# Performance work log

Measured on AMD Instinct MI355X. Metric: run time of the kernel, lower is better.

The kernel has to match this reference:

```python
import jax, jax.numpy as jnp
import numpy as np

N = 10000          # nodes
E = 320000         # edges (avg degree 32)
D_IN = 64          # node_pos feature width
NS, NG, NV = 128, 128, 128   # gate: scalars, gates, gated channels
NTYPES = 8         # edge types
FC = 64            # fc_neurons hidden width
D_OUT = 64
NUM_NEIGHBORS = 32.0


def setup_inputs() -> dict:
    key = jax.random.key(0)
    ks = jax.random.split(key, 32)
    inp = {}
    inp["node_pos"] = jax.random.normal(ks[0], (N, D_IN), dtype=jnp.float32)
    dims_in = [D_IN, D_IN + NS + NV, D_IN + NS + NV]     # 64, 320, 320
    dims_out = [NS + NG + NV, NS + NG + NV, D_OUT]       # 384, 384, 64
    i = 1
    for l in range(3):
        di, do = dims_in[l], dims_out[l]
        inp[f"w_self_{l}"] = jax.random.normal(ks[i], (di, do), dtype=jnp.float32) / np.sqrt(di); i += 1
        inp[f"w_msg_{l}"] = jax.random.normal(ks[i], (di, do), dtype=jnp.float32) / np.sqrt(di); i += 1
        inp[f"fc0_{l}"] = jax.random.normal(ks[i], (NTYPES, FC), dtype=jnp.float32) / np.sqrt(NTYPES); i += 1
        inp[f"fc1_{l}"] = jax.random.normal(ks[i], (FC, FC), dtype=jnp.float32) / np.sqrt(FC); i += 1
        inp[f"fc2_{l}"] = jax.random.normal(ks[i], (FC, do), dtype=jnp.float32) / np.sqrt(FC); i += 1
    inp["edge_src"] = jax.random.randint(ks[i], (E,), 0, N); i += 1
    inp["edge_dst"] = jax.random.randint(ks[i], (E,), 0, N); i += 1
    inp["edge_type"] = jax.random.randint(ks[i], (E,), 0, NTYPES)
    return inp


def _conv(x, edge_src, edge_dst, etype_onehot, w_self, w_msg, f0, f1, f2):
    # fc_neurons MLP on edge attrs -> per-edge tensor-product weights [E, out]
    w = jax.nn.silu(etype_onehot @ f0)
    w = jax.nn.silu(w @ f1)
    w = w @ f2
    # gather source node features, weighted message, scatter-sum to dst
    msg = (x[edge_src] @ w_msg) * w                       # [E, out]
    agg = jax.ops.segment_sum(msg, edge_dst, num_segments=N)
    agg = agg / jnp.sqrt(jnp.asarray(NUM_NEIGHBORS, x.dtype))
    return x @ w_self + agg                               # self-connection + messages


def _gate(h):
    # e3nn Gate: scalars -> silu, gates -> sigmoid, gated channels modulated by gates
    s = h[:, :NS]
    g = h[:, NS:NS + NG]
    v = h[:, NS + NG:]
    return jnp.concatenate([jax.nn.silu(s), v * jax.nn.sigmoid(g)], axis=-1)


def reference(node_pos,
              w_self_0, w_msg_0, fc0_0, fc1_0, fc2_0,
              w_self_1, w_msg_1, fc0_1, fc1_1, fc2_1,
              w_self_2, w_msg_2, fc0_2, fc1_2, fc2_2,
              edge_src, edge_dst, edge_type):
    etype_onehot = jax.nn.one_hot(edge_type, NTYPES, dtype=node_pos.dtype)
    mid = node_pos
    params = [(w_self_0, w_msg_0, fc0_0, fc1_0, fc2_0),
              (w_self_1, w_msg_1, fc0_1, fc1_1, fc2_1)]
    for w_self, w_msg, f0, f1, f2 in params:
        h = _conv(mid, edge_src, edge_dst, etype_onehot, w_self, w_msg, f0, f1, f2)
        mid = jnp.concatenate([node_pos, _gate(h)], axis=-1)   # concated_tensor
    return _conv(mid, edge_src, edge_dst, etype_onehot, w_self_2, w_msg_2, fc0_2, fc1_2, fc2_2)
```

## Files before the change

### kernel.cpp

```cpp
#include <hip/hip_runtime.h>
#include <hip/hip_bf16.h>

#define N_NODES 10000
#define N_EDGES 320000
#define NTYPES 8
#define FC 64
#define SLOTS 96

using short8v = __attribute__((ext_vector_type(8))) short;
using f32x4   = __attribute__((ext_vector_type(4))) float;

__device__ __forceinline__ float sigmoidf_(float x) { return 1.f / (1.f + expf(-x)); }

__device__ __forceinline__ unsigned short f2bf(float x) {
    union { float f; unsigned u; } un; un.f = x;
    unsigned r = un.u + 0x7fff + ((un.u >> 16) & 1);
    return (unsigned short)(r >> 16);
}
__device__ __forceinline__ float bf2f(unsigned short b) {
    union { unsigned u; float f; } un; un.u = ((unsigned)b) << 16;
    return un.f;
}
__device__ __forceinline__ float bflo(unsigned d) {
    union { unsigned u; float f; } un; un.u = d << 16; return un.f;
}
__device__ __forceinline__ float bfhi(unsigned d) {
    union { unsigned u; float f; } un; un.u = d & 0xffff0000u; return un.f;
}
__device__ __forceinline__ unsigned packbf(float lo, float hi) {
    return (unsigned)f2bf(lo) | ((unsigned)f2bf(hi) << 16);
}

__device__ __forceinline__ void wtrans(const float* __restrict__ in,
                                       unsigned short* __restrict__ out,
                                       int K, int Nn, int idx) {
    int n = idx / K, k = idx - n * K;
    out[idx] = f2bf(in[k * Nn + n]);
}

__global__ void prep_misc(const float* __restrict__ node_pos,
                          const float* __restrict__ w0, const float* __restrict__ w1,
                          const float* __restrict__ w2, const float* __restrict__ w3,
                          const float* __restrict__ w4, const float* __restrict__ w5,
                          int* __restrict__ cnt, unsigned short* __restrict__ np16,
                          unsigned short* __restrict__ o0, unsigned short* __restrict__ o1,
                          unsigned short* __restrict__ o2, unsigned short* __restrict__ o3,
                          unsigned short* __restrict__ o4, unsigned short* __restrict__ o5) {
    int idx = blockIdx.x * 256 + threadIdx.x;
    if (idx < N_NODES) { cnt[idx] = 0; return; }
    idx -= N_NODES;
    if (idx < N_NODES * 64) { np16[idx] = f2bf(node_pos[idx]); return; }
    idx -= N_NODES * 64;
    if (idx < 24576) { wtrans(w0, o0, 64, 384, idx); return; }
    idx -= 24576;
    if (idx < 24576) { wtrans(w1, o1, 64, 384, idx); return; }
    idx -= 24576;
    if (idx < 122880) { wtrans(w2, o2, 320, 384, idx); return; }
    idx -= 122880;
    if (idx < 122880) { wtrans(w3, o3, 320, 384, idx); return; }
    idx -= 122880;
    if (idx < 20480) { wtrans(w4, o4, 320, 64, idx); return; }
    idx -= 20480;
    if (idx < 20480) { wtrans(w5, o5, 320, 64, idx); return; }
}
#define PREP_TOTAL (N_NODES + N_NODES * 64 + 2 * 24576 + 2 * 122880 + 2 * 20480)

__global__ void fill_kernel(const int* __restrict__ esrc, const int* __restrict__ edst,
                            const int* __restrict__ etype, int* __restrict__ cnt,
                            int* __restrict__ csr) {
    int e = blockIdx.x * 256 + threadIdx.x;
    if (e >= N_EDGES) return;
    int d = edst[e];
    int pos = atomicAdd(&cnt[d], 1);
    if (pos < SLOTS) csr[d * SLOTS + pos] = esrc[e] * 8 + etype[e];
}

__global__ void wtab_fused(const float* __restrict__ f0_0, const float* __restrict__ f1_0,
                           const float* __restrict__ f2_0,
                           const float* __restrict__ f0_1, const float* __restrict__ f1_1,
                           const float* __restrict__ f2_1,
                           const float* __restrict__ f0_2, const float* __restrict__ f1_2,
                           const float* __restrict__ f2_2,
                           float* __restrict__ wtab0, float* __restrict__ wtab1,
                           float* __restrict__ wtab2) {
    const int tid = threadIdx.x;
    const int bb = blockIdx.x;
    const float *f0, *f1, *f2;
    float* wtab;
    int dout, idx;
    if (bb < 12)      { f0 = f0_0; f1 = f1_0; f2 = f2_0; wtab = wtab0; dout = 384; idx = bb * 256 + tid; }
    else if (bb < 24) { f0 = f0_1; f1 = f1_1; f2 = f2_1; wtab = wtab1; dout = 384; idx = (bb - 12) * 256 + tid; }
    else              { f0 = f0_2; f1 = f1_2; f2 = f2_2; wtab = wtab2; dout = 64;  idx = (bb - 24) * 256 + tid; }
    __shared__ float a[NTYPES * FC];
    __shared__ float bs[NTYPES * FC];
    for (int i = tid; i < NTYPES * FC; i += 256) { float v = f0[i]; a[i] = v * sigmoidf_(v); }
    __syncthreads();
    for (int i = tid; i < NTYPES * FC; i += 256) {
        int t = i >> 6, j = i & 63;
        float s = 0.f;
        #pragma unroll
        for (int k = 0; k < FC; ++k) s = fmaf(a[t * FC + k], f1[k * FC + j], s);
        bs[i] = s * sigmoidf_(s);
    }
    __syncthreads();
    if (idx >= NTYPES * dout) return;
    int t = idx / dout, c = idx - t * dout;
    float s = 0.f;
    #pragma unroll
    for (int k = 0; k < FC; ++k) s = fmaf(bs[t * FC + k], f2[k * dout + c], s);
    wtab[idx] = s * 0.17677669529663687f;
}

__global__ __launch_bounds__(256) void mfma_dual(
        const unsigned short* __restrict__ A,
        const unsigned short* __restrict__ BtS, const unsigned short* __restrict__ BtM,
        float* __restrict__ Cs, unsigned short* __restrict__ Cm,
        int M, int K, int N, int nct) {
    int by = blockIdx.y;
    const bool is_msg = (by >= nct);
    const unsigned short* Bt = is_msg ? BtM : BtS;
    if (is_msg) by -= nct;
    const int wave = threadIdx.x >> 6;
    const int lane = threadIdx.x & 63;
    const int r16 = lane & 15;
    const int kg  = lane >> 4;
    const int rowBase = blockIdx.x * 128 + wave * 32;
    const int colBase = by * 64;

    f32x4 acc[2][4] = {};
    for (int k0 = 0; k0 < K; k0 += 32) {
        short8v a[2], b[4];
        #pragma unroll
        for (int mi = 0; mi < 2; ++mi) {
            int r = rowBase + mi * 16 + r16;
            if (r >= M) r = M - 1;
            a[mi] = *reinterpret_cast<const short8v*>(&A[(long long)r * K + k0 + kg * 8]);
        }
        #pragma unroll
        for (int nj = 0; nj < 4; ++nj) {
            int c = colBase + nj * 16 + r16;
            b[nj] = *reinterpret_cast<const short8v*>(&Bt[(long long)c * K + k0 + kg * 8]);
        }
        #pragma unroll
        for (int mi = 0; mi < 2; ++mi)
            #pragma unroll
            for (int nj = 0; nj < 4; ++nj)
                acc[mi][nj] = __builtin_amdgcn_mfma_f32_16x16x32_bf16(
                                  a[mi], b[nj], acc[mi][nj], 0, 0, 0);
    }
    #pragma unroll
    for (int mi = 0; mi < 2; ++mi) {
        #pragma unroll
        for (int j = 0; j < 4; ++j) {
            int r = rowBase + mi * 16 + kg * 4 + j;
            if (r >= M) continue;
            #pragma unroll
            for (int nj = 0; nj < 4; ++nj) {
                int c = colBase + nj * 16 + r16;
                float v = acc[mi][nj][j];
                if (is_msg) Cm[(long long)r * N + c] = f2bf(v);
                else        Cs[(long long)r * N + c] = v;
            }
        }
    }
}

__global__ void gather_gate(const unsigned short* __restrict__ ymsg,
                            const float* __restrict__ yself,
                            const unsigned short* __restrict__ np16,
                            const float* __restrict__ wtab,
                            const int* __restrict__ cnt,
                            const int* __restrict__ csr,
                            unsigned short* __restrict__ mid16) {
    __shared__ float wt[NTYPES * 384];
    const int tid = threadIdx.x;
    for (int i = tid; i < NTYPES * 384; i += 256) wt[i] = wtab[i];
    __syncthreads();
    const int node = blockIdx.x * 4 + (tid >> 6);
    const int lane = tid & 63;
    if (node >= N_NODES) return;
    int deg = cnt[node];
    if (deg > SLOTS) deg = SLOTS;
    const int* __restrict__ row = csr + node * SLOTS;
    const unsigned* __restrict__ y32 = (const unsigned*)ymsg;
    const float2* __restrict__ wt2 = (const float2*)wt;
    float acc[3][2] = {};
    int i = 0;
    for (; i + 3 < deg; i += 4) {
        int p0 = row[i], p1 = row[i + 1], p2 = row[i + 2], p3 = row[i + 3];
        unsigned b0 = (unsigned)(p0 >> 3) * 192u + lane, t0 = (unsigned)(p0 & 7) * 192u + lane;
        unsigned b1 = (unsigned)(p1 >> 3) * 192u + lane, t1 = (unsigned)(p1 & 7) * 192u + lane;
        unsigned b2 = (unsigned)(p2 >> 3) * 192u + lane, t2 = (unsigned)(p2 & 7) * 192u + lane;
        unsigned b3 = (unsigned)(p3 >> 3) * 192u + lane, t3 = (unsigned)(p3 & 7) * 192u + lane;
        #pragma unroll
        for (int j = 0; j < 3; ++j) {
            const unsigned o = j * 64;
            unsigned d0 = y32[b0 + o]; float2 w0 = wt2[t0 + o];
            unsigned d1 = y32[b1 + o]; float2 w1 = wt2[t1 + o];
            unsigned d2 = y32[b2 + o]; float2 w2 = wt2[t2 + o];
            unsigned d3 = y32[b3 + o]; float2 w3 = wt2[t3 + o];
            acc[j][0] = fmaf(bflo(d0), w0.x, acc[j][0]);
            acc[j][1] = fmaf(bfhi(d0), w0.y, acc[j][1]);
            acc[j][0] = fmaf(bflo(d1), w1.x, acc[j][0]);
            acc[j][1] = fmaf(bfhi(d1), w1.y, acc[j][1]);
            acc[j][0] = fmaf(bflo(d2), w2.x, acc[j][0]);
            acc[j][1] = fmaf(bfhi(d2), w2.y, acc[j][1]);
            acc[j][0] = fmaf(bflo(d3), w3.x, acc[j][0]);
            acc[j][1] = fmaf(bfhi(d3), w3.y, acc[j][1]);
        }
    }
    for (; i < deg; ++i) {
        int p0 = row[i];
        unsigned b0 = (unsigned)(p0 >> 3) * 192u + lane, t0 = (unsigned)(p0 & 7) * 192u + lane;
        #pragma unroll
        for (int j = 0; j < 3; ++j) {
            unsigned d0 = y32[b0 + j * 64]; float2 w0 = wt2[t0 + j * 64];
            acc[j][0] = fmaf(bflo(d0), w0.x, acc[j][0]);
            acc[j][1] = fmaf(bfhi(d0), w0.y, acc[j][1]);
        }
    }
    const float2* __restrict__ ysv = (const float2*)(yself + (long long)node * 384);
    float h[3][2];
    #pragma unroll
    for (int j = 0; j < 3; ++j) {
        float2 ys = ysv[j * 64 + lane];
        h[j][0] = ys.x + acc[j][0];
        h[j][1] = ys.y + acc[j][1];
    }
    unsigned* __restrict__ m32 = (unsigned*)(mid16 + (long long)node * 320);
    const unsigned* __restrict__ np32 = (const unsigned*)np16;
    if (lane < 32) m32[lane] = np32[node * 32 + lane];
    m32[32 + lane] = packbf(h[0][0] * sigmoidf_(h[0][0]),
                            h[0][1] * sigmoidf_(h[0][1]));
    m32[96 + lane] = packbf(h[2][0] * sigmoidf_(h[1][0]),
                            h[2][1] * sigmoidf_(h[1][1]));
}

__global__ void gather_final(const unsigned short* __restrict__ ymsg,
                             const float* __restrict__ yself,
                             const float* __restrict__ wtab,
                             const int* __restrict__ cnt,
                             const int* __restrict__ csr,
                             float* __restrict__ out) {
    __shared__ float wt[NTYPES * 64];
    const int tid = threadIdx.x;
    for (int i = tid; i < NTYPES * 64; i += 256) wt[i] = wtab[i];
    __syncthreads();
    const int node = blockIdx.x * 4 + (tid >> 6);
    const int lane = tid & 63;
    if (node >= N_NODES) return;
    int deg = cnt[node];
    if (deg > SLOTS) deg = SLOTS;
    const int* __restrict__ row = csr + node * SLOTS;
    const unsigned* __restrict__ y32 = (const unsigned*)ymsg;
    const float2* __restrict__ wt2 = (const float2*)wt;
    const int half = lane >> 5, cl = lane & 31;
    float a0 = 0.f, a1 = 0.f;
    int i = 0;
    for (; i + 7 < deg; i += 8) {
        #pragma unroll
        for (int q = 0; q < 4; ++q) {
            int p = row[i + 2 * q + half];
            unsigned d = y32[(unsigned)(p >> 3) * 32u + cl];
            float2 w = wt2[(unsigned)(p & 7) * 32u + cl];
            a0 = fmaf(bflo(d), w.x, a0);
            a1 = fmaf(bfhi(d), w.y, a1);
        }
    }
    for (; i + 1 < deg; i += 2) {
        int p = row[i + half];
        unsigned d = y32[(unsigned)(p >> 3) * 32u + cl];
        float2 w = wt2[(unsigned)(p & 7) * 32u + cl];
        a0 = fmaf(bflo(d), w.x, a0);
        a1 = fmaf(bfhi(d), w.y, a1);
    }
    if (i < deg) {
        if (half == 0) {
            int p = row[i];
            unsigned d = y32[(unsigned)(p >> 3) * 32u + cl];
            float2 w = wt2[(unsigned)(p & 7) * 32u + cl];
            a0 = fmaf(bflo(d), w.x, a0);
            a1 = fmaf(bfhi(d), w.y, a1);
        }
    }
    a0 += __shfl_xor(a0, 32);
    a1 += __shfl_xor(a1, 32);
    if (half == 0) {
        float2 o;
        o.x = yself[(long long)node * 64 + 2 * cl]     + a0;
        o.y = yself[(long long)node * 64 + 2 * cl + 1] + a1;
        reinterpret_cast<float2*>(out)[(long long)node * 32 + cl] = o;
    }
}

extern "C" void kernel_launch(void* const* d_in, const int* in_sizes, int n_in,
                              void* d_out, int out_size, void* d_ws, size_t ws_size,
                              hipStream_t stream) {
    const float* node_pos = (const float*)d_in[0];
    const float* w_self[3] = {(const float*)d_in[1], (const float*)d_in[6],  (const float*)d_in[11]};
    const float* w_msg[3]  = {(const float*)d_in[2], (const float*)d_in[7],  (const float*)d_in[12]};
    const float* fc0[3]    = {(const float*)d_in[3], (const float*)d_in[8],  (const float*)d_in[13]};
    const float* fc1[3]    = {(const float*)d_in[4], (const float*)d_in[9],  (const float*)d_in[14]};
    const float* fc2[3]    = {(const float*)d_in[5], (const float*)d_in[10], (const float*)d_in[15]};
    const int* esrc  = (const int*)d_in[16];
    const int* edst  = (const int*)d_in[17];
    const int* etype = (const int*)d_in[18];
    float* out = (float*)d_out;

    float* f = (float*)d_ws;
    float* wtab0 = f; f += NTYPES * 384;
    float* wtab1 = f; f += NTYPES * 384;
    float* wtab2 = f; f += NTYPES * 64;
    float* yself = f; f += (long long)N_NODES * 384;
    unsigned short* u = (unsigned short*)f;
    unsigned short* ymsg16 = u; u += (long long)N_NODES * 384;
    unsigned short* mid16  = u; u += (long long)N_NODES * 320;
    unsigned short* np16   = u; u += (long long)N_NODES * 64;
    unsigned short* bt0s = u; u += 64 * 384;
    unsigned short* bt0m = u; u += 64 * 384;
    unsigned short* bt1s = u; u += 320 * 384;
    unsigned short* bt1m = u; u += 320 * 384;
    unsigned short* bt2s = u; u += 320 * 64;
    unsigned short* bt2m = u; u += 320 * 64;
    int* ip = (int*)u;
    int* cnt = ip; ip += N_NODES;
    int* csr = ip; ip += (long long)N_NODES * SLOTS;

    prep_misc<<<(PREP_TOTAL + 255) / 256, 256, 0, stream>>>(
        node_pos, w_self[0], w_msg[0], w_self[1], w_msg[1], w_self[2], w_msg[2],
        cnt, np16, bt0s, bt0m, bt1s, bt1m, bt2s, bt2m);

    fill_kernel<<<(N_EDGES + 255) / 256, 256, 0, stream>>>(esrc, edst, etype, cnt, csr);

    wtab_fused<<<26, 256, 0, stream>>>(fc0[0], fc1[0], fc2[0],
                                       fc0[1], fc1[1], fc2[1],
                                       fc0[2], fc1[2], fc2[2],
                                       wtab0, wtab1, wtab2);

    const int ggrid_n = (N_NODES + 3) / 4;
    const int mrows = (N_NODES + 127) / 128;

    {
        dim3 g(mrows, 2 * (384 / 64));
        mfma_dual<<<g, 256, 0, stream>>>(np16, bt0s, bt0m, yself, ymsg16,
                                         N_NODES, 64, 384, 384 / 64);
        gather_gate<<<ggrid_n, 256, 0, stream>>>(ymsg16, yself, np16, wtab0, cnt, csr, mid16);
    }
    {
        dim3 g(mrows, 2 * (384 / 64));
        mfma_dual<<<g, 256, 0, stream>>>(mid16, bt1s, bt1m, yself, ymsg16,
                                         N_NODES, 320, 384, 384 / 64);
        gather_gate<<<ggrid_n, 256, 0, stream>>>(ymsg16, yself, np16, wtab1, cnt, csr, mid16);
    }
    {
        dim3 g(mrows, 2 * (64 / 64));
        mfma_dual<<<g, 256, 0, stream>>>(mid16, bt2s, bt2m, yself, ymsg16,
                                         N_NODES, 320, 64, 64 / 64);
        gather_final<<<ggrid_n, 256, 0, stream>>>(ymsg16, yself, wtab2, cnt, csr, out);
    }
}
```

Before: 180.1 us.

## Split gather-gate by channel chunk with XCD-aware block mapping; merge prep kernels

The gather_gate kernel is split into three channel chunks (scalars, and two gate+value halves). Block IDs are mapped so that each XCD handles one chunk of one node range, which lets each XCD's L2 cache hold a narrower slice of the message matrix. Each block now loads only a 64-entry slice of the weight table into shared memory. The wtab kernel is merged into the prep kernel, and fill_kernel now handles four edges per thread with vector loads. The cost is triple the CSR and index traffic, plus a hard-coded mapping from block ID to XCD.

```diff
diff --git a/kernel.cpp b/kernel.cpp
--- a/kernel.cpp
+++ b/kernel.cpp
@@ -17,10 +17,6 @@
     unsigned r = un.u + 0x7fff + ((un.u >> 16) & 1);
     return (unsigned short)(r >> 16);
 }
-__device__ __forceinline__ float bf2f(unsigned short b) {
-    union { unsigned u; float f; } un; un.u = ((unsigned)b) << 16;
-    return un.f;
-}
 __device__ __forceinline__ float bflo(unsigned d) {
     union { unsigned u; float f; } un; un.u = d << 16; return un.f;
 }
@@ -38,15 +34,54 @@
     out[idx] = f2bf(in[k * Nn + n]);
 }
 
-__global__ void prep_misc(const float* __restrict__ node_pos,
-                          const float* __restrict__ w0, const float* __restrict__ w1,
-                          const float* __restrict__ w2, const float* __restrict__ w3,
-                          const float* __restrict__ w4, const float* __restrict__ w5,
-                          int* __restrict__ cnt, unsigned short* __restrict__ np16,
-                          unsigned short* __restrict__ o0, unsigned short* __restrict__ o1,
-                          unsigned short* __restrict__ o2, unsigned short* __restrict__ o3,
-                          unsigned short* __restrict__ o4, unsigned short* __restrict__ o5) {
-    int idx = blockIdx.x * 256 + threadIdx.x;
+#define PREP_TOTAL (N_NODES + N_NODES * 64 + 2 * 24576 + 2 * 122880 + 2 * 20480)
+
+__global__ void prep_all(const float* __restrict__ node_pos,
+                         const float* __restrict__ w0, const float* __restrict__ w1,
+                         const float* __restrict__ w2, const float* __restrict__ w3,
+                         const float* __restrict__ w4, const float* __restrict__ w5,
+                         const float* __restrict__ f0_0, const float* __restrict__ f1_0,
+                         const float* __restrict__ f2_0,
+                         const float* __restrict__ f0_1, const float* __restrict__ f1_1,
+                         const float* __restrict__ f2_1,
+                         const float* __restrict__ f0_2, const float* __restrict__ f1_2,
+                         const float* __restrict__ f2_2,
+                         int* __restrict__ cnt, unsigned short* __restrict__ np16,
+                         unsigned short* __restrict__ o0, unsigned short* __restrict__ o1,
+                         unsigned short* __restrict__ o2, unsigned short* __restrict__ o3,
+                         unsigned short* __restrict__ o4, unsigned short* __restrict__ o5,
+                         float* __restrict__ wtab0, float* __restrict__ wtab1,
+                         float* __restrict__ wtab2) {
+    const int tid = threadIdx.x;
+    const int bb = blockIdx.x;
+    if (bb < 26) {
+        const float *f0, *f1, *f2;
+        float* wtab;
+        int dout, idx;
+        if (bb < 12)      { f0 = f0_0; f1 = f1_0; f2 = f2_0; wtab = wtab0; dout = 384; idx = bb * 256 + tid; }
+        else if (bb < 24) { f0 = f0_1; f1 = f1_1; f2 = f2_1; wtab = wtab1; dout = 384; idx = (bb - 12) * 256 + tid; }
+        else              { f0 = f0_2; f1 = f1_2; f2 = f2_2; wtab = wtab2; dout = 64;  idx = (bb - 24) * 256 + tid; }
+        __shared__ float a[NTYPES * FC];
+        __shared__ float bs[NTYPES * FC];
+        for (int i = tid; i < NTYPES * FC; i += 256) { float v = f0[i]; a[i] = v * sigmoidf_(v); }
+        __syncthreads();
+        for (int i = tid; i < NTYPES * FC; i += 256) {
+            int t = i >> 6, j = i & 63;
+            float s = 0.f;
+            #pragma unroll
+            for (int k = 0; k < FC; ++k) s = fmaf(a[t * FC + k], f1[k * FC + j], s);
+            bs[i] = s * sigmoidf_(s);
+        }
+        __syncthreads();
+        if (idx >= NTYPES * dout) return;
+        int t = idx / dout, c = idx - t * dout;
+        float s = 0.f;
+        #pragma unroll
+        for (int k = 0; k < FC; ++k) s = fmaf(bs[t * FC + k], f2[k * dout + c], s);
+        wtab[idx] = s * 0.17677669529663687f;
+        return;
+    }
+    int idx = (bb - 26) * 256 + tid;
     if (idx < N_NODES) { cnt[idx] = 0; return; }
     idx -= N_NODES;
     if (idx < N_NODES * 64) { np16[idx] = f2bf(node_pos[idx]); return; }
@@ -63,52 +98,20 @@
     idx -= 20480;
     if (idx < 20480) { wtrans(w5, o5, 320, 64, idx); return; }
 }
-#define PREP_TOTAL (N_NODES + N_NODES * 64 + 2 * 24576 + 2 * 122880 + 2 * 20480)
 
 __global__ void fill_kernel(const int* __restrict__ esrc, const int* __restrict__ edst,
                             const int* __restrict__ etype, int* __restrict__ cnt,
                             int* __restrict__ csr) {
-    int e = blockIdx.x * 256 + threadIdx.x;
-    if (e >= N_EDGES) return;
-    int d = edst[e];
-    int pos = atomicAdd(&cnt[d], 1);
-    if (pos < SLOTS) csr[d * SLOTS + pos] = esrc[e] * 8 + etype[e];
-}
-
-__global__ void wtab_fused(const float* __restrict__ f0_0, const float* __restrict__ f1_0,
-                           const float* __restrict__ f2_0,
-                           const float* __restrict__ f0_1, const float* __restrict__ f1_1,
-                           const float* __restrict__ f2_1,
-                           const float* __restrict__ f0_2, const float* __restrict__ f1_2,
-                           const float* __restrict__ f2_2,
-                           float* __restrict__ wtab0, float* __restrict__ wtab1,
-                           float* __restrict__ wtab2) {
-    const int tid = threadIdx.x;
-    const int bb = blockIdx.x;
-    const float *f0, *f1, *f2;
-    float* wtab;
-    int dout, idx;
-    if (bb < 12)      { f0 = f0_0; f1 = f1_0; f2 = f2_0; wtab = wtab0; dout = 384; idx = bb * 256 + tid; }
-    else if (bb < 24) { f0 = f0_1; f1 = f1_1; f2 = f2_1; wtab = wtab1; dout = 384; idx = (bb - 12) * 256 + tid; }
-    else              { f0 = f0_2; f1 = f1_2; f2 = f2_2; wtab = wtab2; dout = 64;  idx = (bb - 24) * 256 + tid; }
-    __shared__ float a[NTYPES * FC];
-    __shared__ float bs[NTYPES * FC];
-    for (int i = tid; i < NTYPES * FC; i += 256) { float v = f0[i]; a[i] = v * sigmoidf_(v); }
-    __syncthreads();
-    for (int i = tid; i < NTYPES * FC; i += 256) {
-        int t = i >> 6, j = i & 63;
-        float s = 0.f;
-        #pragma unroll
-        for (int k = 0; k < FC; ++k) s = fmaf(a[t * FC + k], f1[k * FC + j], s);
-        bs[i] = s * sigmoidf_(s);
-    }
-    __syncthreads();
-    if (idx >= NTYPES * dout) return;
-    int t = idx / dout, c = idx - t * dout;
-    float s = 0.f;
-    #pragma unroll
-    for (int k = 0; k < FC; ++k) s = fmaf(bs[t * FC + k], f2[k * dout + c], s);
-    wtab[idx] = s * 0.17677669529663687f;
+    int e4 = (blockIdx.x * 256 + threadIdx.x) * 4;
+    if (e4 >= N_EDGES) return;
+    int4 s = *reinterpret_cast<const int4*>(&esrc[e4]);
+    int4 d = *reinterpret_cast<const int4*>(&edst[e4]);
+    int4 t = *reinterpret_cast<const int4*>(&etype[e4]);
+    int p;
+    p = atomicAdd(&cnt[d.x], 1); if (p < SLOTS) csr[d.x * SLOTS + p] = s.x * 8 + t.x;
+    p = atomicAdd(&cnt[d.y], 1); if (p < SLOTS) csr[d.y * SLOTS + p] = s.y * 8 + t.y;
+    p = atomicAdd(&cnt[d.z], 1); if (p < SLOTS) csr[d.z * SLOTS + p] = s.z * 8 + t.z;
+    p = atomicAdd(&cnt[d.w], 1); if (p < SLOTS) csr[d.w * SLOTS + p] = s.w * 8 + t.w;
 }
 
 __global__ __launch_bounds__(256) void mfma_dual(
@@ -165,75 +168,92 @@
     }
 }
 
-__global__ void gather_gate(const unsigned short* __restrict__ ymsg,
-                            const float* __restrict__ yself,
-                            const unsigned short* __restrict__ np16,
-                            const float* __restrict__ wtab,
-                            const int* __restrict__ cnt,
-                            const int* __restrict__ csr,
-                            unsigned short* __restrict__ mid16) {
-    __shared__ float wt[NTYPES * 384];
+__device__ __forceinline__ int dwmap(int c, int l) {
+    if (c == 0) return l;
+    if (c == 1) return (l < 32) ? 64 + l : 96 + l;
+    return (l < 32) ? 96 + l : 128 + l;
+}
+
+__global__ __launch_bounds__(256) void gather_gate3(
+        const unsigned short* __restrict__ ymsg,
+        const float* __restrict__ yself,
+        const unsigned short* __restrict__ np16,
+        const float* __restrict__ wtab,
+        const int* __restrict__ cnt,
+        const int* __restrict__ csr,
+        unsigned short* __restrict__ mid16) {
+    const int id = blockIdx.x;
+    const int xcd = id & 7, widx = id >> 3;
+    int c, o;
+    if (xcd < 6) { c = xcd - (xcd >= 3 ? 3 : 0); o = (xcd >= 3); }
+    else if (xcd == 6) { c = 2; o = 2; }
+    else { c = 1; o = 2; }
+    int nodeblk;
+    if (c == 0) {
+        if (widx >= 1250) return;
+        nodeblk = o * 1250 + widx;
+    } else {
+        int q = (o < 2) ? 834 : 832;
+        if (widx >= q) return;
+        nodeblk = o * 834 + widx;
+    }
+
     const int tid = threadIdx.x;
-    for (int i = tid; i < NTYPES * 384; i += 256) wt[i] = wtab[i];
+    const int lane = tid & 63;
+    const int dwl = dwmap(c, lane);
+
+    __shared__ float2 wt_loc[NTYPES * 64];
+    const float2* __restrict__ wt2 = (const float2*)wtab;
+    for (int i = tid; i < NTYPES * 64; i += 256) {
+        int t = i >> 6, l = i & 63;
+        wt_loc[i] = wt2[t * 192 + dwmap(c, l)];
+    }
     __syncthreads();
-    const int node = blockIdx.x * 4 + (tid >> 6);
-    const int lane = tid & 63;
-    if (node >= N_NODES) return;
+
+    const int node = nodeblk * 4 + (tid >> 6);
     int deg = cnt[node];
     if (deg > SLOTS) deg = SLOTS;
     const int* __restrict__ row = csr + node * SLOTS;
     const unsigned* __restrict__ y32 = (const unsigned*)ymsg;
-    const float2* __restrict__ wt2 = (const float2*)wt;
-    float acc[3][2] = {};
+    float a0 = 0.f, a1 = 0.f;
     int i = 0;
     for (; i + 3 < deg; i += 4) {
-        int p0 = row[i], p1 = row[i + 1], p2 = row[i + 2], p3 = row[i + 3];
-        unsigned b0 = (unsigned)(p0 >> 3) * 192u + lane, t0 = (unsigned)(p0 & 7) * 192u + lane;
-        unsigned b1 = (unsigned)(p1 >> 3) * 192u + lane, t1 = (unsigned)(p1 & 7) * 192u + lane;
-        unsigned b2 = (unsigned)(p2 >> 3) * 192u + lane, t2 = (unsigned)(p2 & 7) * 192u + lane;
-        unsigned b3 = (unsigned)(p3 >> 3) * 192u + lane, t3 = (unsigned)(p3 & 7) * 192u + lane;
-        #pragma unroll
-        for (int j = 0; j < 3; ++j) {
-            const unsigned o = j * 64;
-            unsigned d0 = y32[b0 + o]; float2 w0 = wt2[t0 + o];
-            unsigned d1 = y32[b1 + o]; float2 w1 = wt2[t1 + o];
-            unsigned d2 = y32[b2 + o]; float2 w2 = wt2[t2 + o];
-            unsigned d3 = y32[b3 + o]; float2 w3 = wt2[t3 + o];
-            acc[j][0] = fmaf(bflo(d0), w0.x, acc[j][0]);
-            acc[j][1] = fmaf(bfhi(d0), w0.y, acc[j][1]);
-            acc[j][0] = fmaf(bflo(d1), w1.x, acc[j][0]);
-            acc[j][1] = fmaf(bfhi(d1), w1.y, acc[j][1]);
-            acc[j][0] = fmaf(bflo(d2), w2.x, acc[j][0]);
-            acc[j][1] = fmaf(bfhi(d2), w2.y, acc[j][1]);
-            acc[j][0] = fmaf(bflo(d3), w3.x, acc[j][0]);
-            acc[j][1] = fmaf(bfhi(d3), w3.y, acc[j][1]);
-        }
+        int4 p = *reinterpret_cast<const int4*>(&row[i]);
+        unsigned d0 = y32[(unsigned)(p.x >> 3) * 192u + dwl]; float2 w0 = wt_loc[(p.x & 7) * 64 + lane];
+        unsigned d1 = y32[(unsigned)(p.y >> 3) * 192u + dwl]; float2 w1 = wt_loc[(p.y & 7) * 64 + lane];
+        unsigned d2 = y32[(unsigned)(p.z >> 3) * 192u + dwl]; float2 w2 = wt_loc[(p.z & 7) * 64 + lane];
+        unsigned d3 = y32[(unsigned)(p.w >> 3) * 192u + dwl]; float2 w3 = wt_loc[(p.w & 7) * 64 + lane];
+        a0 = fmaf(bflo(d0), w0.x, a0);  a1 = fmaf(bfhi(d0), w0.y, a1);
+        a0 = fmaf(bflo(d1), w1.x, a0);  a1 = fmaf(bfhi(d1), w1.y, a1);
+        a0 = fmaf(bflo(d2), w2.x, a0);  a1 = fmaf(bfhi(d2), w2.y, a1);
+        a0 = fmaf(bflo(d3), w3.x, a0);  a1 = fmaf(bfhi(d3), w3.y, a1);
     }
     for (; i < deg; ++i) {
         int p0 = row[i];
-        unsigned b0 = (unsigned)(p0 >> 3) * 192u + lane, t0 = (unsigned)(p0 & 7) * 192u + lane;
-        #pragma unroll
-        for (int j = 0; j < 3; ++j) {
-            unsigned d0 = y32[b0 + j * 64]; float2 w0 = wt2[t0 + j * 64];
-            acc[j][0] = fmaf(bflo(d0), w0.x, acc[j][0]);
-            acc[j][1] = fmaf(bfhi(d0), w0.y, acc[j][1]);
-        }
-    }
-    const float2* __restrict__ ysv = (const float2*)(yself + (long long)node * 384);
-    float h[3][2];
-    #pragma unroll
-    for (int j = 0; j < 3; ++j) {
-        float2 ys = ysv[j * 64 + lane];
-        h[j][0] = ys.x + acc[j][0];
-        h[j][1] = ys.y + acc[j][1];
-    }
+        unsigned d0 = y32[(unsigned)(p0 >> 3) * 192u + dwl];
+        float2 w0 = wt_loc[(p0 & 7) * 64 + lane];
+        a0 = fmaf(bflo(d0), w0.x, a0);  a1 = fmaf(bfhi(d0), w0.y, a1);
+    }
+    const float2* __restrict__ ysv = (const float2*)yself;
+    float2 ys = ysv[(long long)node * 192 + dwl];
+    float h0 = ys.x + a0, h1 = ys.y + a1;
+
     unsigned* __restrict__ m32 = (unsigned*)(mid16 + (long long)node * 320);
-    const unsigned* __restrict__ np32 = (const unsigned*)np16;
-    if (lane < 32) m32[lane] = np32[node * 32 + lane];
-    m32[32 + lane] = packbf(h[0][0] * sigmoidf_(h[0][0]),
-                            h[0][1] * sigmoidf_(h[0][1]));
-    m32[96 + lane] = packbf(h[2][0] * sigmoidf_(h[1][0]),
-                            h[2][1] * sigmoidf_(h[1][1]));
+    if (c == 0) {
+        m32[32 + lane] = packbf(h0 * sigmoidf_(h0), h1 * sigmoidf_(h1));
+        if (lane < 32) {
+            const unsigned* __restrict__ np32 = (const unsigned*)np16;
+            m32[lane] = np32[node * 32 + lane];
+        }
+    } else {
+        float g0 = __shfl_xor(h0, 32);
+        float g1 = __shfl_xor(h1, 32);
+        if (lane >= 32) {
+            int l2 = lane - 32;
+            m32[(c == 1 ? 96 : 128) + l2] = packbf(h0 * sigmoidf_(g0),
+                                                   h1 * sigmoidf_(g1));
+        }
+    }
 }
 
 __global__ void gather_final(const unsigned short* __restrict__ ymsg,
@@ -326,36 +346,31 @@
     int* cnt = ip; ip += N_NODES;
     int* csr = ip; ip += (long long)N_NODES * SLOTS;
 
-    prep_misc<<<(PREP_TOTAL + 255) / 256, 256, 0, stream>>>(
+    prep_all<<<26 + (PREP_TOTAL + 255) / 256, 256, 0, stream>>>(
         node_pos, w_self[0], w_msg[0], w_self[1], w_msg[1], w_self[2], w_msg[2],
-        cnt, np16, bt0s, bt0m, bt1s, bt1m, bt2s, bt2m);
-
-    fill_kernel<<<(N_EDGES + 255) / 256, 256, 0, stream>>>(esrc, edst, etype, cnt, csr);
-
-    wtab_fused<<<26, 256, 0, stream>>>(fc0[0], fc1[0], fc2[0],
-                                       fc0[1], fc1[1], fc2[1],
-                                       fc0[2], fc1[2], fc2[2],
-                                       wtab0, wtab1, wtab2);
-
-    const int ggrid_n = (N_NODES + 3) / 4;
+        fc0[0], fc1[0], fc2[0], fc0[1], fc1[1], fc2[1], fc0[2], fc1[2], fc2[2],
+        cnt, np16, bt0s, bt0m, bt1s, bt1m, bt2s, bt2m, wtab0, wtab1, wtab2);
+
+    fill_kernel<<<(N_EDGES / 4 + 255) / 256, 256, 0, stream>>>(esrc, edst, etype, cnt, csr);
+
     const int mrows = (N_NODES + 127) / 128;
 
     {
         dim3 g(mrows, 2 * (384 / 64));
         mfma_dual<<<g, 256, 0, stream>>>(np16, bt0s, bt0m, yself, ymsg16,
                                          N_NODES, 64, 384, 384 / 64);
-        gather_gate<<<ggrid_n, 256, 0, stream>>>(ymsg16, yself, np16, wtab0, cnt, csr, mid16);
+        gather_gate3<<<10000, 256, 0, stream>>>(ymsg16, yself, np16, wtab0, cnt, csr, mid16);
     }
     {
         dim3 g(mrows, 2 * (384 / 64));
         mfma_dual<<<g, 256, 0, stream>>>(mid16, bt1s, bt1m, yself, ymsg16,
                                          N_NODES, 320, 384, 384 / 64);
-        gather_gate<<<ggrid_n, 256, 0, stream>>>(ymsg16, yself, np16, wtab1, cnt, csr, mid16);
+        gather_gate3<<<10000, 256, 0, stream>>>(ymsg16, yself, np16, wtab1, cnt, csr, mid16);
     }
     {
         dim3 g(mrows, 2 * (64 / 64));
         mfma_dual<<<g, 256, 0, stream>>>(mid16, bt2s, bt2m, yself, ymsg16,
                                          N_NODES, 320, 64, 64 / 64);
-        gather_final<<<ggrid_n, 256, 0, stream>>>(ymsg16, yself, wtab2, cnt, csr, out);
-    }
-}
+        gather_final<<<(N_NODES + 3) / 4, 256, 0, stream>>>(ymsg16, yself, wtab2, cnt, csr, out);
+    }
+}
```

New measurement: 205.6 us. 1.14x slower.
